# Kernel tuning notes

Hardware: AMD Instinct MI355X
Metric: run time of the kernel (lower is better)

## Reference

```python
import jax, jax.numpy as jnp
import numpy as np

BATCH = 32      # init batch_size
HID = 256       # init hidden_dim
SENT = 64       # sentence_size
WORDS = 64      # words per sentence (the -1 in the view)
N = BATCH * SENT


def setup_inputs() -> dict:
    key = jax.random.key(0)
    k1, k2, k3, k4 = jax.random.split(key, 4)
    stdv_lin = 1.0 / np.sqrt(HID)
    x = jax.random.normal(k1, (N, WORDS, HID), dtype=jnp.float32)
    W = jax.random.uniform(k2, (HID, HID), jnp.float32, -stdv_lin, stdv_lin)
    b = jax.random.uniform(k3, (HID,), jnp.float32, -stdv_lin, stdv_lin)
    context = jax.random.uniform(k4, (HID,), jnp.float32, -stdv_lin, stdv_lin)
    return {"x": x, "W": W, "b": b, "context": context, "sentence_size": SENT}


def reference(x, W, b, context, sentence_size):
    # tanh(Linear(x)) applied per position; vectorized over the batch loop
    attends = jnp.tanh(jnp.einsum("nwh,oh->nwo", x, W) + b)  # [N, WORDS, HID]
    scores = attends * context                                 # [N, WORDS, HID]
    # nn.Softmax on the [-1, HID] view -> softmax over the hidden dim
    alpha = jax.nn.softmax(scores, axis=-1)                    # [N, WORDS, HID]
    attended = x * alpha                                       # legacy same-numel mul
    attended = attended.reshape(BATCH, sentence_size, -1, HID)
    return jnp.sum(attended, axis=2)                           # [BATCH, SENT, HID]
```

## Files before the change

kernel.cpp:

```cpp
#include <hip/hip_runtime.h>
#include <hip/hip_bf16.h>

#define HID 256
#define NROWS 2048
#define NITER 8
#define GRID (NROWS / NITER)
#define PITCH 264
#define AS1 __attribute__((address_space(1)))
#define AS3 __attribute__((address_space(3)))

typedef __attribute__((ext_vector_type(8))) short short8;
typedef __attribute__((ext_vector_type(4))) float float4v;
typedef __attribute__((ext_vector_type(4))) unsigned short ushort4v;

__device__ __forceinline__ float bf2f(unsigned short u) {
    return __uint_as_float(((unsigned int)u) << 16);
}

__device__ __forceinline__ unsigned int pk_bf16(float a, float b) {
    __hip_bfloat162 p = __float22bfloat162_rn(float2{a, b});
    return *(unsigned int*)&p;
}

__device__ __forceinline__ float tanh_fast(float x) {
    float e = __builtin_amdgcn_exp2f(x * 2.8853900817779268f);
    return 1.0f - 2.0f * __builtin_amdgcn_rcpf(e + 1.0f);
}

__device__ __forceinline__ float exp_small(float s) {
    float p = __builtin_fmaf(s, 0.16666667f, 0.5f);
    p = __builtin_fmaf(p, s, 1.0f);
    return __builtin_fmaf(p, s, 1.0f);
}

__global__ void cvt_w(const float* __restrict__ W, unsigned short* __restrict__ Wb) {
    int i = blockIdx.x * 256 + threadIdx.x;
    float4v v = ((const float4v*)W)[i];
    unsigned int lo = pk_bf16(v.x, v.y), hi = pk_bf16(v.z, v.w);
    ushort4v u;
    u.x = (unsigned short)lo; u.y = (unsigned short)(lo >> 16);
    u.z = (unsigned short)hi; u.w = (unsigned short)(hi >> 16);
    ((ushort4v*)Wb)[i] = u;
}

__global__ __launch_bounds__(512, 2) void attend_fused(
    const float* __restrict__ x, const unsigned short* __restrict__ Wb,
    const float* __restrict__ bias, const float* __restrict__ ctx,
    float* __restrict__ out)
{
    __shared__ float fstage[64 * 256];
    __shared__ unsigned short xs[64 * PITCH];
    __shared__ float wsum[8][64];
    __shared__ float rinv[64];

    const int tid  = threadIdx.x;
    const int wave = tid >> 6;
    const int lane = tid & 63;
    const int q    = lane >> 4;
    const int c    = lane & 15;
    const int obase = wave * 32;

    float bb[2], cc[2];
#pragma unroll
    for (int nt = 0; nt < 2; ++nt) {
        bb[nt] = bias[obase + nt * 16 + c];
        cc[nt] = ctx[obase + nt * 16 + c];
    }
    short8 bfrag[8][2];
#pragma unroll
    for (int nt = 0; nt < 2; ++nt) {
        const unsigned short* wr = &Wb[(size_t)(obase + nt * 16 + c) * 256 + q * 8];
#pragma unroll
        for (int kt = 0; kt < 8; ++kt)
            bfrag[kt][nt] = *(const short8*)(wr + kt * 32);
    }

    const int n0 = blockIdx.x * NITER;

    {
        const float* xn = x + (size_t)n0 * (64 * 256);
#pragma unroll
        for (int t = 0; t < 8; ++t) {
            const int row = wave * 8 + t;
            __builtin_amdgcn_global_load_lds((const AS1 void*)(xn + row * 256 + lane * 4),
                                             (AS3 void*)&fstage[row * 256], 16, 0, 0);
        }
    }

    for (int it = 0; it < NITER; ++it) {
        const int n = n0 + it;
        __syncthreads();

#pragma unroll
        for (int i = 0; i < 8; ++i) {
            const int chunk = tid + 512 * i;
            const int r = chunk >> 6, col4 = (chunk & 63) * 4;
            float4v v = *(const float4v*)&fstage[chunk * 4];
            uint2 u;
            u.x = pk_bf16(v.x, v.y);
            u.y = pk_bf16(v.z, v.w);
            *(uint2*)&xs[r * PITCH + col4] = u;
        }
        __syncthreads();

        if (it + 1 < NITER) {
            const float* xn = x + (size_t)(n + 1) * (64 * 256);
#pragma unroll
            for (int t = 0; t < 8; ++t) {
                const int row = wave * 8 + t;
                __builtin_amdgcn_global_load_lds((const AS1 void*)(xn + row * 256 + lane * 4),
                                                 (AS3 void*)&fstage[row * 256], 16, 0, 0);
            }
        }

        float4v acc[4][2];
#pragma unroll
        for (int mt = 0; mt < 4; ++mt)
#pragma unroll
            for (int nt = 0; nt < 2; ++nt)
                acc[mt][nt] = (float4v){0.f, 0.f, 0.f, 0.f};

#pragma unroll
        for (int kt = 0; kt < 8; ++kt) {
            short8 a[4];
#pragma unroll
            for (int mt = 0; mt < 4; ++mt)
                a[mt] = *(const short8*)&xs[(mt * 16 + c) * PITCH + kt * 32 + q * 8];
#pragma unroll
            for (int nt = 0; nt < 2; ++nt)
#pragma unroll
                for (int mt = 0; mt < 4; ++mt)
                    acc[mt][nt] = __builtin_amdgcn_mfma_f32_16x16x32_bf16(
                        a[mt], bfrag[kt][nt], acc[mt][nt], 0, 0, 0);
        }

        float psum[4][4];
#pragma unroll
        for (int mt = 0; mt < 4; ++mt)
#pragma unroll
            for (int r = 0; r < 4; ++r)
                psum[mt][r] = 0.f;

#pragma unroll
        for (int nt = 0; nt < 2; ++nt) {
#pragma unroll
            for (int mt = 0; mt < 4; ++mt) {
#pragma unroll
                for (int r = 0; r < 4; ++r) {
                    float s = tanh_fast(acc[mt][nt][r] + bb[nt]) * cc[nt];
                    float e = exp_small(s);
                    acc[mt][nt][r] = e;
                    psum[mt][r] += e;
                }
            }
        }
#pragma unroll
        for (int mt = 0; mt < 4; ++mt)
#pragma unroll
            for (int r = 0; r < 4; ++r) {
                float v = psum[mt][r];
                v += __shfl_xor(v, 1);
                v += __shfl_xor(v, 2);
                v += __shfl_xor(v, 4);
                v += __shfl_xor(v, 8);
                psum[mt][r] = v;
            }
        if (c == 0) {
#pragma unroll
            for (int mt = 0; mt < 4; ++mt)
#pragma unroll
                for (int r = 0; r < 4; ++r)
                    wsum[wave][mt * 16 + q * 4 + r] = psum[mt][r];
        }
        __syncthreads();
        if (tid < 64) {
            float t = wsum[0][tid] + wsum[1][tid] + wsum[2][tid] + wsum[3][tid]
                    + wsum[4][tid] + wsum[5][tid] + wsum[6][tid] + wsum[7][tid];
            rinv[tid] = __builtin_amdgcn_rcpf(t);
        }
        __syncthreads();

        float ri[4][4];
#pragma unroll
        for (int mt = 0; mt < 4; ++mt)
#pragma unroll
            for (int r = 0; r < 4; ++r)
                ri[mt][r] = rinv[mt * 16 + q * 4 + r];

        float outp[2] = {0.f, 0.f};
#pragma unroll
        for (int nt = 0; nt < 2; ++nt) {
            const int h = obase + nt * 16 + c;
#pragma unroll
            for (int mt = 0; mt < 4; ++mt) {
#pragma unroll
                for (int r = 0; r < 4; ++r) {
                    const int w = mt * 16 + q * 4 + r;
                    outp[nt] += bf2f(xs[w * PITCH + h]) * (acc[mt][nt][r] * ri[mt][r]);
                }
            }
        }
#pragma unroll
        for (int nt = 0; nt < 2; ++nt) {
            float v = outp[nt];
            v += __shfl_xor(v, 16);
            v += __shfl_xor(v, 32);
            if (q == 0)
                out[(size_t)n * HID + obase + nt * 16 + c] = v;
        }
    }
}

extern "C" void kernel_launch(void* const* d_in, const int* in_sizes, int n_in,
                              void* d_out, int out_size, void* d_ws, size_t ws_size,
                              hipStream_t stream) {
    const float* x    = (const float*)d_in[0];
    const float* W    = (const float*)d_in[1];
    const float* bias = (const float*)d_in[2];
    const float* ctx  = (const float*)d_in[3];
    unsigned short* Wb = (unsigned short*)d_ws;

    cvt_w<<<64, 256, 0, stream>>>(W, Wb);
    attend_fused<<<GRID, 512, 0, stream>>>(x, Wb, bias, ctx, (float*)d_out);
}
```

Baseline: 207.8 us.

## Interleave output columns, use DPP row reductions, and split next-tile prefetch

Each lane now owns two adjacent output columns (2c, 2c+1) rather than columns c and c+16. This lets the epilogue read x as one 32-bit bf16 pair and write the output as a float2. The 16-lane softmax sum switches from shfl_xor to DPP row operations. The global-to-LDS prefetch of the next tile is split into two halves issued at different points, to spread memory traffic around the MFMA and the barriers. Risks include LDS bank conflicts from the new access pattern and possible row-mask errors in the DPP control values.

```diff
diff --git a/kernel.cpp b/kernel.cpp
--- a/kernel.cpp
+++ b/kernel.cpp
@@ -31,6 +31,23 @@
     float p = __builtin_fmaf(s, 0.16666667f, 0.5f);
     p = __builtin_fmaf(p, s, 1.0f);
     return __builtin_fmaf(p, s, 1.0f);
+}
+
+__device__ __forceinline__ float row16_sum(float v) {
+    float t;
+    t = __builtin_bit_cast(float, __builtin_amdgcn_update_dpp(
+            0, __builtin_bit_cast(int, v), 0xB1, 0xf, 0xf, true));
+    v += t;
+    t = __builtin_bit_cast(float, __builtin_amdgcn_update_dpp(
+            0, __builtin_bit_cast(int, v), 0x4E, 0xf, 0xf, true));
+    v += t;
+    t = __builtin_bit_cast(float, __builtin_amdgcn_update_dpp(
+            0, __builtin_bit_cast(int, v), 0x124, 0xf, 0xf, true));
+    v += t;
+    t = __builtin_bit_cast(float, __builtin_amdgcn_update_dpp(
+            0, __builtin_bit_cast(int, v), 0x128, 0xf, 0xf, true));
+    v += t;
+    return v;
 }
 
 __global__ void cvt_w(const float* __restrict__ W, unsigned short* __restrict__ Wb) {
@@ -63,13 +80,13 @@
     float bb[2], cc[2];
 #pragma unroll
     for (int nt = 0; nt < 2; ++nt) {
-        bb[nt] = bias[obase + nt * 16 + c];
-        cc[nt] = ctx[obase + nt * 16 + c];
+        bb[nt] = bias[obase + 2 * c + nt];
+        cc[nt] = ctx[obase + 2 * c + nt];
     }
     short8 bfrag[8][2];
 #pragma unroll
     for (int nt = 0; nt < 2; ++nt) {
-        const unsigned short* wr = &Wb[(size_t)(obase + nt * 16 + c) * 256 + q * 8];
+        const unsigned short* wr = &Wb[(size_t)(obase + 2 * c + nt) * 256 + q * 8];
 #pragma unroll
         for (int kt = 0; kt < 8; ++kt)
             bfrag[kt][nt] = *(const short8*)(wr + kt * 32);
@@ -89,6 +106,9 @@
 
     for (int it = 0; it < NITER; ++it) {
         const int n = n0 + it;
+        const float* xnext = x + (size_t)(n + 1) * (64 * 256);
+        const bool pf = (it + 1 < NITER);
+
         __syncthreads();
 
 #pragma unroll
@@ -103,12 +123,11 @@
         }
         __syncthreads();
 
-        if (it + 1 < NITER) {
-            const float* xn = x + (size_t)(n + 1) * (64 * 256);
-#pragma unroll
-            for (int t = 0; t < 8; ++t) {
+        if (pf) {
+#pragma unroll
+            for (int t = 0; t < 4; ++t) {
                 const int row = wave * 8 + t;
-                __builtin_amdgcn_global_load_lds((const AS1 void*)(xn + row * 256 + lane * 4),
+                __builtin_amdgcn_global_load_lds((const AS1 void*)(xnext + row * 256 + lane * 4),
                                                  (AS3 void*)&fstage[row * 256], 16, 0, 0);
             }
         }
@@ -157,14 +176,8 @@
 #pragma unroll
         for (int mt = 0; mt < 4; ++mt)
 #pragma unroll
-            for (int r = 0; r < 4; ++r) {
-                float v = psum[mt][r];
-                v += __shfl_xor(v, 1);
-                v += __shfl_xor(v, 2);
-                v += __shfl_xor(v, 4);
-                v += __shfl_xor(v, 8);
-                psum[mt][r] = v;
-            }
+            for (int r = 0; r < 4; ++r)
+                psum[mt][r] = row16_sum(psum[mt][r]);
         if (c == 0) {
 #pragma unroll
             for (int mt = 0; mt < 4; ++mt)
@@ -180,6 +193,15 @@
         }
         __syncthreads();
 
+        if (pf) {
+#pragma unroll
+            for (int t = 4; t < 8; ++t) {
+                const int row = wave * 8 + t;
+                __builtin_amdgcn_global_load_lds((const AS1 void*)(xnext + row * 256 + lane * 4),
+                                                 (AS3 void*)&fstage[row * 256], 16, 0, 0);
+            }
+        }
+
         float ri[4][4];
 #pragma unroll
         for (int mt = 0; mt < 4; ++mt)
@@ -189,15 +211,14 @@
 
         float outp[2] = {0.f, 0.f};
 #pragma unroll
-        for (int nt = 0; nt < 2; ++nt) {
-            const int h = obase + nt * 16 + c;
-#pragma unroll
-            for (int mt = 0; mt < 4; ++mt) {
-#pragma unroll
-                for (int r = 0; r < 4; ++r) {
-                    const int w = mt * 16 + q * 4 + r;
-                    outp[nt] += bf2f(xs[w * PITCH + h]) * (acc[mt][nt][r] * ri[mt][r]);
-                }
+        for (int mt = 0; mt < 4; ++mt) {
+#pragma unroll
+            for (int r = 0; r < 4; ++r) {
+                const int w = mt * 16 + q * 4 + r;
+                unsigned int pair = *(const unsigned int*)&xs[w * PITCH + obase + 2 * c];
+                const float wgt = ri[mt][r];
+                outp[0] += bf2f((unsigned short)pair)         * (acc[mt][0][r] * wgt);
+                outp[1] += bf2f((unsigned short)(pair >> 16)) * (acc[mt][1][r] * wgt);
             }
         }
 #pragma unroll
@@ -205,9 +226,10 @@
             float v = outp[nt];
             v += __shfl_xor(v, 16);
             v += __shfl_xor(v, 32);
-            if (q == 0)
-                out[(size_t)n * HID + obase + nt * 16 + c] = v;
-        }
+            outp[nt] = v;
+        }
+        if (q == 0)
+            *(float2*)&out[(size_t)n * HID + obase + 2 * c] = float2{outp[0], outp[1]};
     }
 }
 
```

Result: no change. 205.8 us (-1.0%).
